# Kernel optimization log

Measured on AMD Instinct MI355X. Metric: run time of the kernel, lower is better.

The kernel has to match this reference:

```python
import jax, jax.numpy as jnp
import numpy as np

CUTOFF = 5.0

def ssp(x):
    # shifted softplus: ln(0.5*e^x + 0.5)
    return jax.nn.softplus(x) - jnp.log(2.0).astype(x.dtype)

def cosine_cutoff(r):
    return 0.5 * (jnp.cos(jnp.pi * r / CUTOFF) + 1.0) * (r < CUTOFF).astype(r.dtype)

def setup_inputs() -> dict:
    key = jax.random.key(0)
    ks = jax.random.split(key, 16)
    B, A, N, Nd, F, Din, Dout, Th = 2, 512, 1024, 64, 64, 128, 128, 25
    inp = {}
    inp['x'] = jax.random.normal(ks[0], (B, A, Din), dtype=jnp.float32)
    inp['r_double'] = jax.random.uniform(ks[1], (B, A, Nd), dtype=jnp.float32)
    inp['r_ij'] = jax.random.uniform(ks[2], (B, A, N), dtype=jnp.float32)
    inp['r_ik'] = jax.random.uniform(ks[3], (B, A, N), dtype=jnp.float32)
    inp['r_jk'] = jax.random.uniform(ks[4], (B, A, N), dtype=jnp.float32)
    inp['neighbors'] = jax.random.randint(ks[5], (B, A, Nd), 0, A, dtype=jnp.int32)
    inp['neighbor_mask'] = jnp.ones((B, A, Nd), dtype=jnp.float32)
    inp['neighbors_j'] = jax.random.randint(ks[6], (B, A, N), 0, A, dtype=jnp.int32)
    inp['neighbors_k'] = jax.random.randint(ks[7], (B, A, N), 0, A, dtype=jnp.int32)
    inp['triple_masks'] = jnp.ones((B, A, N), dtype=jnp.float32)
    inp['d_ijk'] = jax.random.uniform(ks[8], (B, A, N, Th), dtype=jnp.float32)
    s = 0.1
    inp['W_in2f'] = s * jax.random.normal(ks[9], (Din, F), dtype=jnp.float32)
    inp['W_t1'] = s * jax.random.normal(ks[10], (Th, F), dtype=jnp.float32)
    inp['b_t1'] = jnp.zeros((F,), dtype=jnp.float32)
    inp['W_t2'] = s * jax.random.normal(ks[11], (F, F), dtype=jnp.float32)
    inp['b_t2'] = jnp.zeros((F,), dtype=jnp.float32)
    inp['W_f2out'] = s * jax.random.normal(ks[12], (F, Dout), dtype=jnp.float32)
    inp['b_f2out'] = jnp.zeros((Dout,), dtype=jnp.float32)
    return inp

def reference(x, r_double, r_ij, r_ik, r_jk, neighbors, neighbor_mask,
              neighbors_j, neighbors_k, triple_masks, d_ijk,
              W_in2f, W_t1, b_t1, W_t2, b_t2, W_f2out, b_f2out):
    # Triple filter: 2-layer MLP on angular basis, modulated by cutoffs
    h = ssp(jnp.einsum('bant,tf->banf', d_ijk, W_t1) + b_t1)
    W_triple = jnp.einsum('banf,fg->bang', h, W_t2) + b_t2
    W_triple = W_triple * cosine_cutoff(r_ij)[..., None] * cosine_cutoff(r_ik)[..., None]

    # in2f: (B, A, F)
    y = jnp.einsum('bad,df->baf', x, W_in2f)
    B, A, N = neighbors_j.shape
    F = y.shape[-1]
    # gather neighbor features along atom axis
    yj = jnp.take_along_axis(y, neighbors_j.reshape(B, A * N, 1), axis=1).reshape(B, A, N, F)
    yk = jnp.take_along_axis(y, neighbors_k.reshape(B, A * N, 1), axis=1).reshape(B, A, N, F)
    w_ij = r_ij[..., None]
    w_ik = r_ik[..., None]
    y = (w_ij * yj + w_ik * yk) / (w_ij + w_ik)
    # filter multiply + masked sum aggregation over triples axis
    y = y * W_triple
    y = jnp.sum(y * triple_masks[..., None], axis=2)
    # f2out with shifted-softplus activation
    out = ssp(jnp.einsum('baf,fo->bao', y, W_f2out) + b_f2out)
    return out
```

## Files before the change

### kernel.cpp

```cpp
#include <hip/hip_runtime.h>
#include <hip/hip_fp16.h>

#define BB 2
#define AA 512
#define NN 1024
#define FF 64
#define DIN 128
#define DOUT 128
#define TH 25
#define ASTRIDE 40
#define HSTRIDE 72
#define NSPLIT 2
#define NIT 8

typedef _Float16 half8 __attribute__((ext_vector_type(8)));
typedef _Float16 half4v __attribute__((ext_vector_type(4)));
typedef float floatx4 __attribute__((ext_vector_type(4)));

#define LOG2E 1.44269504088896f
#define LN2F  0.693147180559945f

__device__ __forceinline__ float ssp_f(float x) {
    return __logf(0.5f * __expf(x) + 0.5f);
}

__device__ __forceinline__ float cutcos(float r) {
    float c = 0.5f * (__cosf(r * (3.14159265358979323846f / 5.0f)) + 1.0f);
    return (r < 5.0f) ? c : 0.0f;
}

__device__ __forceinline__ __half2 ssp2f(__half2 z) {
    const __half2 hlf = __float2half2_rn(0.5f);
    return h2log2(__hadd2(h2exp2(z), hlf));
}

__device__ __forceinline__ __half2 pk2(float a, float b) {
    auto v = __builtin_amdgcn_cvt_pkrtz(a, b);
    __half2 r;
    __builtin_memcpy(&r, &v, sizeof(r));
    return r;
}

__device__ __forceinline__ half4v pack4(__half2 lo, __half2 hi) {
    half4v r;
    __builtin_memcpy(&r, &lo, 4);
    __builtin_memcpy(reinterpret_cast<char*>(&r) + 4, &hi, 4);
    return r;
}

#define OFF_Y       0
#define OFF_PARTIAL (OFF_Y + (size_t)BB * AA * FF * 2)
#define OFF_B1      (OFF_PARTIAL + (size_t)NSPLIT * BB * AA * FF * 4)
#define OFF_B2      (OFF_B1 + 4 * 64 * 8 * 2)
#define OFF_BP      (OFF_B2 + 8 * 64 * 8 * 2)

__global__ void in2f_prep_kernel(const float* __restrict__ x,
                                 const float* __restrict__ Wi,
                                 _Float16* __restrict__ y,
                                 const float* __restrict__ W_t1, const float* __restrict__ b_t1,
                                 const float* __restrict__ W_t2, const float* __restrict__ b_t2,
                                 _Float16* __restrict__ B1tab, _Float16* __restrict__ B2tab,
                                 _Float16* __restrict__ BPtab) {
    __shared__ float xs[DIN];
    const int ba = blockIdx.x;
    const int t = threadIdx.x;
    xs[t] = x[ba * DIN + t];
    xs[t + 64] = x[ba * DIN + 64 + t];
    __syncthreads();
    float acc = 0.f;
#pragma unroll 8
    for (int d = 0; d < DIN; ++d) acc += xs[d] * Wi[d * FF + t];
    y[ba * FF + t] = (_Float16)acc;

    if (ba == 0) {
        const int lane = t, quad = t >> 4, l16 = t & 15;
#pragma unroll
        for (int g = 0; g < 4; ++g) {
            const int featA = g * 16 + l16;
#pragma unroll
            for (int j = 0; j < 8; ++j) {
                int k = quad * 8 + j;
                _Float16 v;
                if (k < TH)       v = (_Float16)(W_t1[k * FF + featA] * LOG2E);
                else if (k == TH) v = (_Float16)(b_t1[featA] * LOG2E - 1.0f);
                else              v = (_Float16)0.f;
                B1tab[(g * 64 + lane) * 8 + j] = v;
            }
#pragma unroll
            for (int e = 0; e < 2; ++e) {
                BPtab[((g * 2 + e) * 64 + lane) * 2 + 0] =
                    (_Float16)b_t2[g * 16 + quad * 4 + 2 * e];
                BPtab[((g * 2 + e) * 64 + lane) * 2 + 1] =
                    (_Float16)b_t2[g * 16 + quad * 4 + 2 * e + 1];
            }
#pragma unroll
            for (int q = 0; q < 2; ++q)
#pragma unroll
                for (int j = 0; j < 8; ++j)
                    B2tab[((g * 2 + q) * 64 + lane) * 8 + j] =
                        (_Float16)(W_t2[(q * 32 + quad * 8 + j) * FF + g * 16 + l16] * LN2F);
        }
    }
}

__global__ __launch_bounds__(256) void triple_kernel(
    const int* __restrict__ nbrj, const int* __restrict__ nbrk,
    const float* __restrict__ r_ij, const float* __restrict__ r_ik,
    const float* __restrict__ tmask, const float* __restrict__ d_ijk,
    const _Float16* __restrict__ B1tab, const _Float16* __restrict__ B2tab,
    const _Float16* __restrict__ BPtab,
    const _Float16* __restrict__ y_tab, float* __restrict__ partial) {

    __shared__ __align__(16) _Float16 a_tile[4][16 * ASTRIDE];
    __shared__ __align__(16) _Float16 h_tile[4][16 * HSTRIDE];
    __shared__ float red[4][FF];

    const int blk = blockIdx.x;
    const int ba = blk >> 1;
    const int split = blk & 1;
    const int b = ba >> 9;
    const int tid = threadIdx.x;
    const int w = tid >> 6;
    const int lane = tid & 63;
    const int quad = lane >> 4;
    const int l16 = lane & 15;
    const int rA = lane >> 3;
    const int fc = (lane & 7) * 8;

    const long ban = (long)ba * NN;
    const float* dbase = d_ijk + (long)ba * NN * TH;
    const _Float16* yb = y_tab + (long)b * (AA * FF);

    half8 B1[4];
    __half2 b2p[4][2];
#pragma unroll
    for (int g = 0; g < 4; ++g) {
        B1[g] = *(const half8*)(B1tab + (g * 64 + lane) * 8);
#pragma unroll
        for (int e = 0; e < 2; ++e)
            b2p[g][e] = *(const __half2*)(BPtab + ((g * 2 + e) * 64 + lane) * 2);
    }
    const _Float16* b2gp = B2tab + lane * 8;

    const int tile0 = split * 32 + quad * 4 + w;
    const long n0a = ban + (long)tile0 * 16 + l16;
    const long n1a = n0a + 256;
    int pp0, pp1, wp0, wp1;
    {
        const float rij0 = r_ij[n0a], rik0 = r_ik[n0a];
        const float rij1 = r_ij[n1a], rik1 = r_ik[n1a];
        const float iv0 = cutcos(rij0) * cutcos(rik0) * tmask[n0a] / (rij0 + rik0);
        const float iv1 = cutcos(rij1) * cutcos(rik1) * tmask[n1a] / (rij1 + rik1);
        __half2 w0 = pk2(rij0 * iv0, rik0 * iv0);
        __half2 w1 = pk2(rij1 * iv1, rik1 * iv1);
        __builtin_memcpy(&wp0, &w0, 4);
        __builtin_memcpy(&wp1, &w1, 4);
        pp0 = nbrj[n0a] | (nbrk[n0a] << 16);
        pp1 = nbrj[n1a] | (nbrk[n1a] << 16);
    }

    for (int idx = lane; idx < 16 * 7; idx += 64) {
        int r = idx / 7, c = 25 + idx % 7;
        a_tile[w][r * ASTRIDE + c] = (c == 25) ? (_Float16)1.f : (_Float16)0.f;
    }

    int lofs2[3][2];
#pragma unroll
    for (int m = 0; m < 3; ++m)
#pragma unroll
        for (int e = 0; e < 2; ++e) {
            int s = m * 128 + lane * 2 + e;
            int r = s / TH, c = s - r * TH;
            lofs2[m][e] = r * ASTRIDE + c;
        }
    const int tofs = 15 * ASTRIDE + 9 + lane;

    float acc[8];
#pragma unroll
    for (int i = 0; i < 8; ++i) acc[i] = 0.f;
    const floatx4 zero4 = {0.f, 0.f, 0.f, 0.f};

    float2 pA[3];
    float pT = 0.f;
    const float* dp0 = dbase + (long)(split * 32 + w) * 16 * TH;
    {
#pragma unroll
        for (int m = 0; m < 3; ++m) pA[m] = *(const float2*)(dp0 + m * 128 + lane * 2);
        if (lane < 16) pT = dp0[384 + lane];
    }

#pragma unroll 1
    for (int it = 0; it < NIT; ++it) {
        const bool s1 = (it >= 4);
        const int sl0 = (it & 3) * 16 + rA;
        const int sl1 = sl0 + 8;
        const int ppS = s1 ? pp1 : pp0;
        const int wpS = s1 ? wp1 : wp0;
        const int ppa = __shfl(ppS, sl0), ppb = __shfl(ppS, sl1);
        const int wpa = __shfl(wpS, sl0), wpb = __shfl(wpS, sl1);
        const int pj0 = ppa & 0xffff, pk0 = ((unsigned)ppa) >> 16;
        const int pj1 = ppb & 0xffff, pk1 = ((unsigned)ppb) >> 16;
        half8 gj0 = *(const half8*)(yb + pj0 * FF + fc);
        half8 gk0 = *(const half8*)(yb + pk0 * FF + fc);
        half8 gj1 = *(const half8*)(yb + pj1 * FF + fc);
        half8 gk1 = *(const half8*)(yb + pk1 * FF + fc);

#pragma unroll
        for (int m = 0; m < 3; ++m) {
            a_tile[w][lofs2[m][0]] = (_Float16)pA[m].x;
            a_tile[w][lofs2[m][1]] = (_Float16)pA[m].y;
        }
        if (lane < 16) a_tile[w][tofs] = (_Float16)pT;

        if (it + 1 < NIT) {
            const float* dn = dp0 + (it + 1) * 1600;
#pragma unroll
            for (int m = 0; m < 3; ++m) pA[m] = *(const float2*)(dn + m * 128 + lane * 2);
            if (lane < 16) pT = dn[384 + lane];
        }

        __half2 wv0, wv1;
        __builtin_memcpy(&wv0, &wpa, 4);
        __builtin_memcpy(&wv1, &wpb, 4);
        const __half2 wj0 = __half2half2(__low2half(wv0));
        const __half2 wk0 = __half2half2(__high2half(wv0));
        const __half2 wj1 = __half2half2(__low2half(wv1));
        const __half2 wk1 = __half2half2(__high2half(wv1));

        half8 afrag = *(const half8*)&a_tile[w][l16 * ASTRIDE + quad * 8];
#pragma unroll
        for (int g = 0; g < 4; ++g) {
            floatx4 hv = __builtin_amdgcn_mfma_f32_16x16x32_f16(B1[g], afrag, zero4, 0, 0, 0);
            __half2 h01 = ssp2f(pk2(hv[0], hv[1]));
            __half2 h23 = ssp2f(pk2(hv[2], hv[3]));
            *(half4v*)&h_tile[w][l16 * HSTRIDE + g * 16 + quad * 4] = pack4(h01, h23);
        }

        half8 a2q0 = *(const half8*)&h_tile[w][l16 * HSTRIDE + quad * 8];
        half8 a2q1 = *(const half8*)&h_tile[w][l16 * HSTRIDE + 32 + quad * 8];
#pragma unroll
        for (int g = 0; g < 4; ++g) {
            const _Float16* b2it = b2gp;
            asm volatile("" : "+v"(b2it));
            half8 B2g0 = *(const half8*)(b2it + (g * 2 + 0) * 512);
            half8 B2g1 = *(const half8*)(b2it + (g * 2 + 1) * 512);
            floatx4 w2 = __builtin_amdgcn_mfma_f32_16x16x32_f16(B2g0, a2q0, zero4, 0, 0, 0);
            w2 = __builtin_amdgcn_mfma_f32_16x16x32_f16(B2g1, a2q1, w2, 0, 0, 0);
            __half2 f01 = __hadd2(pk2(w2[0], w2[1]), b2p[g][0]);
            __half2 f23 = __hadd2(pk2(w2[2], w2[3]), b2p[g][1]);
            *(half4v*)&h_tile[w][l16 * HSTRIDE + g * 16 + quad * 4] = pack4(f01, f23);
        }
        half8 f0 = *(const half8*)&h_tile[w][rA * HSTRIDE + fc];
        half8 f1 = *(const half8*)&h_tile[w][(8 + rA) * HSTRIDE + fc];

        const __half2* gj0p = (const __half2*)&gj0;
        const __half2* gk0p = (const __half2*)&gk0;
        const __half2* gj1p = (const __half2*)&gj1;
        const __half2* gk1p = (const __half2*)&gk1;
        const __half2* f0p = (const __half2*)&f0;
        const __half2* f1p = (const __half2*)&f1;
#pragma unroll
        for (int p = 0; p < 4; ++p) {
            __half2 fv0 = __hfma2(wj0, gj0p[p], __hmul2(wk0, gk0p[p]));
            __half2 fv1 = __hfma2(wj1, gj1p[p], __hmul2(wk1, gk1p[p]));
            __half2 tot = __hfma2(f1p[p], fv1, __hmul2(f0p[p], fv0));
            acc[2 * p]     += __low2float(tot);
            acc[2 * p + 1] += __high2float(tot);
        }
    }

#pragma unroll
    for (int i = 0; i < 8; ++i) {
        acc[i] += __shfl_xor(acc[i], 8, 64);
        acc[i] += __shfl_xor(acc[i], 16, 64);
        acc[i] += __shfl_xor(acc[i], 32, 64);
    }
    if (lane < 8)
#pragma unroll
        for (int i = 0; i < 8; ++i) red[w][lane * 8 + i] = acc[i];
    __syncthreads();

    if (tid < FF)
        partial[(split * (BB * AA) + ba) * FF + tid] =
            red[0][tid] + red[1][tid] + red[2][tid] + red[3][tid];
}

__global__ void out_kernel(const float* __restrict__ partial,
                           const float* __restrict__ Wf,
                           const float* __restrict__ bf,
                           float* __restrict__ out) {
    __shared__ float yag[FF];
    const int ba = blockIdx.x;
    const int t = threadIdx.x;
    if (t < FF) {
        float s = 0.f;
#pragma unroll
        for (int sp = 0; sp < NSPLIT; ++sp)
            s += partial[(sp * (BB * AA) + ba) * FF + t];
        yag[t] = s;
    }
    __syncthreads();
    float a = bf[t];
#pragma unroll 8
    for (int f = 0; f < FF; ++f) a += yag[f] * Wf[f * DOUT + t];
    out[(long)ba * DOUT + t] = ssp_f(a);
}

extern "C" void kernel_launch(void* const* d_in, const int* in_sizes, int n_in,
                              void* d_out, int out_size, void* d_ws, size_t ws_size,
                              hipStream_t stream) {
    const float* x       = (const float*)d_in[0];
    const float* r_ij    = (const float*)d_in[2];
    const float* r_ik    = (const float*)d_in[3];
    const int*   nbrj    = (const int*)d_in[7];
    const int*   nbrk    = (const int*)d_in[8];
    const float* tmask   = (const float*)d_in[9];
    const float* d_ijk   = (const float*)d_in[10];
    const float* W_in2f  = (const float*)d_in[11];
    const float* W_t1    = (const float*)d_in[12];
    const float* b_t1    = (const float*)d_in[13];
    const float* W_t2    = (const float*)d_in[14];
    const float* b_t2    = (const float*)d_in[15];
    const float* W_f2out = (const float*)d_in[16];
    const float* b_f2out = (const float*)d_in[17];
    float* out = (float*)d_out;

    char* ws = (char*)d_ws;
    _Float16* y      = (_Float16*)(ws + OFF_Y);
    float* partial   = (float*)(ws + OFF_PARTIAL);
    _Float16* B1tab  = (_Float16*)(ws + OFF_B1);
    _Float16* B2tab  = (_Float16*)(ws + OFF_B2);
    _Float16* BPtab  = (_Float16*)(ws + OFF_BP);

    in2f_prep_kernel<<<BB * AA, 64, 0, stream>>>(x, W_in2f, y, W_t1, b_t1,
                                                 W_t2, b_t2, B1tab, B2tab, BPtab);
    triple_kernel<<<BB * AA * NSPLIT, 256, 0, stream>>>(nbrj, nbrk, r_ij, r_ik,
                                                        tmask, d_ijk, B1tab, B2tab,
                                                        BPtab, y, partial);
    out_kernel<<<BB * AA, 128, 0, stream>>>(partial, W_f2out, b_f2out, out);
}
```

Baseline: 249.2 us.

## Keep MLP hidden activations in registers by permuting first-layer feature order

Reorders the first-layer weight columns so the MFMA output fragment directly matches the input operand layout of the second MFMA, removing the h_tile shared-memory round trips. The second-layer weights are now held in registers instead of being reloaded each iteration. The filter output is consumed in MFMA output layout, with the gathered y features loaded per lane to match, and the triple reduction becomes a 16-lane shuffle tree. This adds register pressure (B2 weights, 16 accumulators) and more shuffles in the final reduction.

After: 260.7 us. +4.6%, slower.

```diff
diff --git a/kernel.cpp b/kernel.cpp
--- a/kernel.cpp
+++ b/kernel.cpp
@@ -9,7 +9,6 @@
 #define DOUT 128
 #define TH 25
 #define ASTRIDE 40
-#define HSTRIDE 72
 #define NSPLIT 2
 #define NIT 8
 
@@ -41,10 +40,12 @@
     return r;
 }
 
-__device__ __forceinline__ half4v pack4(__half2 lo, __half2 hi) {
-    half4v r;
-    __builtin_memcpy(&r, &lo, 4);
-    __builtin_memcpy(reinterpret_cast<char*>(&r) + 4, &hi, 4);
+__device__ __forceinline__ half8 pack8(__half2 a, __half2 b, __half2 c, __half2 d) {
+    half8 r;
+    __builtin_memcpy(reinterpret_cast<char*>(&r) + 0,  &a, 4);
+    __builtin_memcpy(reinterpret_cast<char*>(&r) + 4,  &b, 4);
+    __builtin_memcpy(reinterpret_cast<char*>(&r) + 8,  &c, 4);
+    __builtin_memcpy(reinterpret_cast<char*>(&r) + 12, &d, 4);
     return r;
 }
 
@@ -74,15 +75,16 @@
 
     if (ba == 0) {
         const int lane = t, quad = t >> 4, l16 = t & 15;
-#pragma unroll
-        for (int g = 0; g < 4; ++g) {
-            const int featA = g * 16 + l16;
+        const int baseg[4] = {0, 4, 32, 36};
+#pragma unroll
+        for (int g = 0; g < 4; ++g) {
+            const int feat_m = baseg[g] + 8 * (l16 >> 2) + (l16 & 3);
 #pragma unroll
             for (int j = 0; j < 8; ++j) {
                 int k = quad * 8 + j;
                 _Float16 v;
-                if (k < TH)       v = (_Float16)(W_t1[k * FF + featA] * LOG2E);
-                else if (k == TH) v = (_Float16)(b_t1[featA] * LOG2E - 1.0f);
+                if (k < TH)       v = (_Float16)(W_t1[k * FF + feat_m] * LOG2E);
+                else if (k == TH) v = (_Float16)(b_t1[feat_m] * LOG2E - 1.0f);
                 else              v = (_Float16)0.f;
                 B1tab[(g * 64 + lane) * 8 + j] = v;
             }
@@ -112,7 +114,6 @@
     const _Float16* __restrict__ y_tab, float* __restrict__ partial) {
 
     __shared__ __align__(16) _Float16 a_tile[4][16 * ASTRIDE];
-    __shared__ __align__(16) _Float16 h_tile[4][16 * HSTRIDE];
     __shared__ float red[4][FF];
 
     const int blk = blockIdx.x;
@@ -124,23 +125,23 @@
     const int lane = tid & 63;
     const int quad = lane >> 4;
     const int l16 = lane & 15;
-    const int rA = lane >> 3;
-    const int fc = (lane & 7) * 8;
 
     const long ban = (long)ba * NN;
     const float* dbase = d_ijk + (long)ba * NN * TH;
     const _Float16* yb = y_tab + (long)b * (AA * FF);
 
     half8 B1[4];
+    half8 B2[4][2];
     __half2 b2p[4][2];
 #pragma unroll
     for (int g = 0; g < 4; ++g) {
         B1[g] = *(const half8*)(B1tab + (g * 64 + lane) * 8);
+        B2[g][0] = *(const half8*)(B2tab + ((g * 2 + 0) * 64 + lane) * 8);
+        B2[g][1] = *(const half8*)(B2tab + ((g * 2 + 1) * 64 + lane) * 8);
 #pragma unroll
         for (int e = 0; e < 2; ++e)
             b2p[g][e] = *(const __half2*)(BPtab + ((g * 2 + e) * 64 + lane) * 2);
     }
-    const _Float16* b2gp = B2tab + lane * 8;
 
     const int tile0 = split * 32 + quad * 4 + w;
     const long n0a = ban + (long)tile0 * 16 + l16;
@@ -175,9 +176,9 @@
         }
     const int tofs = 15 * ASTRIDE + 9 + lane;
 
-    float acc[8];
-#pragma unroll
-    for (int i = 0; i < 8; ++i) acc[i] = 0.f;
+    float acc[16];
+#pragma unroll
+    for (int i = 0; i < 16; ++i) acc[i] = 0.f;
     const floatx4 zero4 = {0.f, 0.f, 0.f, 0.f};
 
     float2 pA[3];
@@ -192,18 +193,20 @@
 #pragma unroll 1
     for (int it = 0; it < NIT; ++it) {
         const bool s1 = (it >= 4);
-        const int sl0 = (it & 3) * 16 + rA;
-        const int sl1 = sl0 + 8;
+        const int sl = (it & 3) * 16 + l16;
         const int ppS = s1 ? pp1 : pp0;
         const int wpS = s1 ? wp1 : wp0;
-        const int ppa = __shfl(ppS, sl0), ppb = __shfl(ppS, sl1);
-        const int wpa = __shfl(wpS, sl0), wpb = __shfl(wpS, sl1);
-        const int pj0 = ppa & 0xffff, pk0 = ((unsigned)ppa) >> 16;
-        const int pj1 = ppb & 0xffff, pk1 = ((unsigned)ppb) >> 16;
-        half8 gj0 = *(const half8*)(yb + pj0 * FF + fc);
-        half8 gk0 = *(const half8*)(yb + pk0 * FF + fc);
-        half8 gj1 = *(const half8*)(yb + pj1 * FF + fc);
-        half8 gk1 = *(const half8*)(yb + pk1 * FF + fc);
+        const int ppa = __shfl(ppS, sl);
+        const int wpa = __shfl(wpS, sl);
+        const int pj = ppa & 0xffff, pk = ((unsigned)ppa) >> 16;
+        const _Float16* yjb = yb + pj * FF + quad * 4;
+        const _Float16* ykb = yb + pk * FF + quad * 4;
+        half4v yj[4], yk[4];
+#pragma unroll
+        for (int g = 0; g < 4; ++g) {
+            yj[g] = *(const half4v*)(yjb + g * 16);
+            yk[g] = *(const half4v*)(ykb + g * 16);
+        }
 
 #pragma unroll
         for (int m = 0; m < 3; ++m) {
@@ -219,65 +222,53 @@
             if (lane < 16) pT = dn[384 + lane];
         }
 
-        __half2 wv0, wv1;
-        __builtin_memcpy(&wv0, &wpa, 4);
-        __builtin_memcpy(&wv1, &wpb, 4);
-        const __half2 wj0 = __half2half2(__low2half(wv0));
-        const __half2 wk0 = __half2half2(__high2half(wv0));
-        const __half2 wj1 = __half2half2(__low2half(wv1));
-        const __half2 wk1 = __half2half2(__high2half(wv1));
+        __half2 wv;
+        __builtin_memcpy(&wv, &wpa, 4);
+        const __half2 wj = __half2half2(__low2half(wv));
+        const __half2 wk = __half2half2(__high2half(wv));
 
         half8 afrag = *(const half8*)&a_tile[w][l16 * ASTRIDE + quad * 8];
+        __half2 hh[8];
 #pragma unroll
         for (int g = 0; g < 4; ++g) {
             floatx4 hv = __builtin_amdgcn_mfma_f32_16x16x32_f16(B1[g], afrag, zero4, 0, 0, 0);
-            __half2 h01 = ssp2f(pk2(hv[0], hv[1]));
-            __half2 h23 = ssp2f(pk2(hv[2], hv[3]));
-            *(half4v*)&h_tile[w][l16 * HSTRIDE + g * 16 + quad * 4] = pack4(h01, h23);
-        }
-
-        half8 a2q0 = *(const half8*)&h_tile[w][l16 * HSTRIDE + quad * 8];
-        half8 a2q1 = *(const half8*)&h_tile[w][l16 * HSTRIDE + 32 + quad * 8];
-#pragma unroll
-        for (int g = 0; g < 4; ++g) {
-            const _Float16* b2it = b2gp;
-            asm volatile("" : "+v"(b2it));
-            half8 B2g0 = *(const half8*)(b2it + (g * 2 + 0) * 512);
-            half8 B2g1 = *(const half8*)(b2it + (g * 2 + 1) * 512);
-            floatx4 w2 = __builtin_amdgcn_mfma_f32_16x16x32_f16(B2g0, a2q0, zero4, 0, 0, 0);
-            w2 = __builtin_amdgcn_mfma_f32_16x16x32_f16(B2g1, a2q1, w2, 0, 0, 0);
+            hh[2 * g]     = ssp2f(pk2(hv[0], hv[1]));
+            hh[2 * g + 1] = ssp2f(pk2(hv[2], hv[3]));
+        }
+        const half8 a2q0 = pack8(hh[0], hh[1], hh[2], hh[3]);
+        const half8 a2q1 = pack8(hh[4], hh[5], hh[6], hh[7]);
+
+#pragma unroll
+        for (int g = 0; g < 4; ++g) {
+            floatx4 w2 = __builtin_amdgcn_mfma_f32_16x16x32_f16(B2[g][0], a2q0, zero4, 0, 0, 0);
+            w2 = __builtin_amdgcn_mfma_f32_16x16x32_f16(B2[g][1], a2q1, w2, 0, 0, 0);
+            const __half2* yj2 = (const __half2*)&yj[g];
+            const __half2* yk2 = (const __half2*)&yk[g];
             __half2 f01 = __hadd2(pk2(w2[0], w2[1]), b2p[g][0]);
             __half2 f23 = __hadd2(pk2(w2[2], w2[3]), b2p[g][1]);
-            *(half4v*)&h_tile[w][l16 * HSTRIDE + g * 16 + quad * 4] = pack4(f01, f23);
-        }
-        half8 f0 = *(const half8*)&h_tile[w][rA * HSTRIDE + fc];
-        half8 f1 = *(const half8*)&h_tile[w][(8 + rA) * HSTRIDE + fc];
-
-        const __half2* gj0p = (const __half2*)&gj0;
-        const __half2* gk0p = (const __half2*)&gk0;
-        const __half2* gj1p = (const __half2*)&gj1;
-        const __half2* gk1p = (const __half2*)&gk1;
-        const __half2* f0p = (const __half2*)&f0;
-        const __half2* f1p = (const __half2*)&f1;
-#pragma unroll
-        for (int p = 0; p < 4; ++p) {
-            __half2 fv0 = __hfma2(wj0, gj0p[p], __hmul2(wk0, gk0p[p]));
-            __half2 fv1 = __hfma2(wj1, gj1p[p], __hmul2(wk1, gk1p[p]));
-            __half2 tot = __hfma2(f1p[p], fv1, __hmul2(f0p[p], fv0));
-            acc[2 * p]     += __low2float(tot);
-            acc[2 * p + 1] += __high2float(tot);
-        }
-    }
-
-#pragma unroll
-    for (int i = 0; i < 8; ++i) {
-        acc[i] += __shfl_xor(acc[i], 8, 64);
-        acc[i] += __shfl_xor(acc[i], 16, 64);
-        acc[i] += __shfl_xor(acc[i], 32, 64);
-    }
-    if (lane < 8)
-#pragma unroll
-        for (int i = 0; i < 8; ++i) red[w][lane * 8 + i] = acc[i];
+            __half2 fv01 = __hfma2(wj, yj2[0], __hmul2(wk, yk2[0]));
+            __half2 fv23 = __hfma2(wj, yj2[1], __hmul2(wk, yk2[1]));
+            __half2 t01 = __hmul2(f01, fv01);
+            __half2 t23 = __hmul2(f23, fv23);
+            acc[g * 4 + 0] += __low2float(t01);
+            acc[g * 4 + 1] += __high2float(t01);
+            acc[g * 4 + 2] += __low2float(t23);
+            acc[g * 4 + 3] += __high2float(t23);
+        }
+    }
+
+#pragma unroll
+    for (int m = 1; m < 16; m <<= 1)
+#pragma unroll
+        for (int i = 0; i < 16; ++i) acc[i] += __shfl_xor(acc[i], m, 64);
+
+    if (l16 == 0) {
+#pragma unroll
+        for (int g = 0; g < 4; ++g) {
+            floatx4 v = {acc[g * 4 + 0], acc[g * 4 + 1], acc[g * 4 + 2], acc[g * 4 + 3]};
+            *(floatx4*)&red[w][g * 16 + quad * 4] = v;
+        }
+    }
     __syncthreads();
 
     if (tid < FF)
```

## Double-buffer angular tile, hoist B2 fragments into registers, raise MFMA priority

Applied to the files above, without the earlier changes.

Makes the per-wave a_tile a two-stage LDS buffer. The next iteration's d_ijk tile is written while the current one is read, and global prefetch runs two iterations ahead to hide load latency. The B2 weight fragments move from per-iteration global loads into registers loaded once, and s_setprio raises wave priority around the MFMA section. This adds LDS and register pressure, which may reduce occupancy.

Result: faster. 233.0 us (-6.5%).

```diff
diff --git a/kernel.cpp b/kernel.cpp
--- a/kernel.cpp
+++ b/kernel.cpp
@@ -111,7 +111,7 @@
     const _Float16* __restrict__ BPtab,
     const _Float16* __restrict__ y_tab, float* __restrict__ partial) {
 
-    __shared__ __align__(16) _Float16 a_tile[4][16 * ASTRIDE];
+    __shared__ __align__(16) _Float16 a_tile[4][2][16 * ASTRIDE];
     __shared__ __align__(16) _Float16 h_tile[4][16 * HSTRIDE];
     __shared__ float red[4][FF];
 
@@ -132,15 +132,17 @@
     const _Float16* yb = y_tab + (long)b * (AA * FF);
 
     half8 B1[4];
+    half8 B2[4][2];
     __half2 b2p[4][2];
 #pragma unroll
     for (int g = 0; g < 4; ++g) {
         B1[g] = *(const half8*)(B1tab + (g * 64 + lane) * 8);
+        B2[g][0] = *(const half8*)(B2tab + ((g * 2 + 0) * 64 + lane) * 8);
+        B2[g][1] = *(const half8*)(B2tab + ((g * 2 + 1) * 64 + lane) * 8);
 #pragma unroll
         for (int e = 0; e < 2; ++e)
             b2p[g][e] = *(const __half2*)(BPtab + ((g * 2 + e) * 64 + lane) * 2);
     }
-    const _Float16* b2gp = B2tab + lane * 8;
 
     const int tile0 = split * 32 + quad * 4 + w;
     const long n0a = ban + (long)tile0 * 16 + l16;
@@ -161,7 +163,9 @@
 
     for (int idx = lane; idx < 16 * 7; idx += 64) {
         int r = idx / 7, c = 25 + idx % 7;
-        a_tile[w][r * ASTRIDE + c] = (c == 25) ? (_Float16)1.f : (_Float16)0.f;
+        _Float16 v = (c == 25) ? (_Float16)1.f : (_Float16)0.f;
+        a_tile[w][0][r * ASTRIDE + c] = v;
+        a_tile[w][1][r * ASTRIDE + c] = v;
     }
 
     int lofs2[3][2];
@@ -187,10 +191,22 @@
 #pragma unroll
         for (int m = 0; m < 3; ++m) pA[m] = *(const float2*)(dp0 + m * 128 + lane * 2);
         if (lane < 16) pT = dp0[384 + lane];
+#pragma unroll
+        for (int m = 0; m < 3; ++m) {
+            a_tile[w][0][lofs2[m][0]] = (_Float16)pA[m].x;
+            a_tile[w][0][lofs2[m][1]] = (_Float16)pA[m].y;
+        }
+        if (lane < 16) a_tile[w][0][tofs] = (_Float16)pT;
+        const float* d1 = dp0 + 1600;
+#pragma unroll
+        for (int m = 0; m < 3; ++m) pA[m] = *(const float2*)(d1 + m * 128 + lane * 2);
+        if (lane < 16) pT = d1[384 + lane];
     }
 
 #pragma unroll 1
     for (int it = 0; it < NIT; ++it) {
+        const int cur = it & 1;
+
         const bool s1 = (it >= 4);
         const int sl0 = (it & 3) * 16 + rA;
         const int sl1 = sl0 + 8;
@@ -205,15 +221,19 @@
         half8 gj1 = *(const half8*)(yb + pj1 * FF + fc);
         half8 gk1 = *(const half8*)(yb + pk1 * FF + fc);
 
-#pragma unroll
-        for (int m = 0; m < 3; ++m) {
-            a_tile[w][lofs2[m][0]] = (_Float16)pA[m].x;
-            a_tile[w][lofs2[m][1]] = (_Float16)pA[m].y;
-        }
-        if (lane < 16) a_tile[w][tofs] = (_Float16)pT;
+        half8 afrag = *(const half8*)&a_tile[w][cur][l16 * ASTRIDE + quad * 8];
 
         if (it + 1 < NIT) {
-            const float* dn = dp0 + (it + 1) * 1600;
+#pragma unroll
+            for (int m = 0; m < 3; ++m) {
+                a_tile[w][cur ^ 1][lofs2[m][0]] = (_Float16)pA[m].x;
+                a_tile[w][cur ^ 1][lofs2[m][1]] = (_Float16)pA[m].y;
+            }
+            if (lane < 16) a_tile[w][cur ^ 1][tofs] = (_Float16)pT;
+        }
+
+        if (it + 2 < NIT) {
+            const float* dn = dp0 + (it + 2) * 1600;
 #pragma unroll
             for (int m = 0; m < 3; ++m) pA[m] = *(const float2*)(dn + m * 128 + lane * 2);
             if (lane < 16) pT = dn[384 + lane];
@@ -227,7 +247,7 @@
         const __half2 wj1 = __half2half2(__low2half(wv1));
         const __half2 wk1 = __half2half2(__high2half(wv1));
 
-        half8 afrag = *(const half8*)&a_tile[w][l16 * ASTRIDE + quad * 8];
+        __builtin_amdgcn_s_setprio(1);
 #pragma unroll
         for (int g = 0; g < 4; ++g) {
             floatx4 hv = __builtin_amdgcn_mfma_f32_16x16x32_f16(B1[g], afrag, zero4, 0, 0, 0);
@@ -240,16 +260,13 @@
         half8 a2q1 = *(const half8*)&h_tile[w][l16 * HSTRIDE + 32 + quad * 8];
 #pragma unroll
         for (int g = 0; g < 4; ++g) {
-            const _Float16* b2it = b2gp;
-            asm volatile("" : "+v"(b2it));
-            half8 B2g0 = *(const half8*)(b2it + (g * 2 + 0) * 512);
-            half8 B2g1 = *(const half8*)(b2it + (g * 2 + 1) * 512);
-            floatx4 w2 = __builtin_amdgcn_mfma_f32_16x16x32_f16(B2g0, a2q0, zero4, 0, 0, 0);
-            w2 = __builtin_amdgcn_mfma_f32_16x16x32_f16(B2g1, a2q1, w2, 0, 0, 0);
+            floatx4 w2 = __builtin_amdgcn_mfma_f32_16x16x32_f16(B2[g][0], a2q0, zero4, 0, 0, 0);
+            w2 = __builtin_amdgcn_mfma_f32_16x16x32_f16(B2[g][1], a2q1, w2, 0, 0, 0);
             __half2 f01 = __hadd2(pk2(w2[0], w2[1]), b2p[g][0]);
             __half2 f23 = __hadd2(pk2(w2[2], w2[3]), b2p[g][1]);
             *(half4v*)&h_tile[w][l16 * HSTRIDE + g * 16 + quad * 4] = pack4(f01, f23);
         }
+        __builtin_amdgcn_s_setprio(0);
         half8 f0 = *(const half8*)&h_tile[w][rA * HSTRIDE + fc];
         half8 f1 = *(const half8*)&h_tile[w][(8 + rA) * HSTRIDE + fc];
 
```
